# Kernel tuning notes

Measured on AMD Instinct MI355X. Metric: run time of the kernel, lower is better.

## Reference

```python
import jax, jax.numpy as jnp
import numpy as np

N, E, D_IN, D_OUT = 100000, 1250000, 64, 100


def setup_inputs() -> dict:
    key = jax.random.key(0)
    ks = jax.random.split(key, 12)
    inp = {
        "x": jax.random.normal(ks[0], (N, D_IN), dtype=jnp.float32),
        "edge_index": jax.random.randint(ks[1], (2, E), 0, N, dtype=jnp.int64),
        "edge_weight": jax.random.uniform(ks[2], (E,), dtype=jnp.float32),
        # ChebConv(64,100,K=1): one weight + bias
        "W10": jax.random.normal(ks[3], (D_IN, D_OUT), dtype=jnp.float32) * 0.1,
        "b1": jnp.zeros((D_OUT,), dtype=jnp.float32),
        # ChebConv(64,100,K=2)
        "W20": jax.random.normal(ks[4], (D_IN, D_OUT), dtype=jnp.float32) * 0.1,
        "W21": jax.random.normal(ks[5], (D_IN, D_OUT), dtype=jnp.float32) * 0.1,
        "b2": jnp.zeros((D_OUT,), dtype=jnp.float32),
        # ChebConv(64,100,K=3)
        "W30": jax.random.normal(ks[6], (D_IN, D_OUT), dtype=jnp.float32) * 0.1,
        "W31": jax.random.normal(ks[7], (D_IN, D_OUT), dtype=jnp.float32) * 0.1,
        "W32": jax.random.normal(ks[8], (D_IN, D_OUT), dtype=jnp.float32) * 0.1,
        "b3": jnp.zeros((D_OUT,), dtype=jnp.float32),
    }
    return inp


def _cheb_norm(edge_index, edge_weight, n):
    # PyG ChebConv.__norm__ with normalization='sym', lambda_max=2.0:
    # L_hat = (2/lambda_max) * (I - D^-1/2 A D^-1/2) - I = -D^-1/2 A D^-1/2
    # (the +1 diagonal of L and the -1 self-loop cancel), diag entries are 0.
    row, col = edge_index[0], edge_index[1]
    deg = jax.ops.segment_sum(edge_weight, row, num_segments=n)
    dis = jnp.where(deg > 0, jax.lax.rsqrt(jnp.where(deg > 0, deg, 1.0)), 0.0)
    return -dis[row] * edge_weight * dis[col]


def _cheb_conv(x, edge_index, w_hat, weights, bias):
    # out = sum_k T_k(L_hat) x @ W_k + b, with T0=x, T1=Lx, T_k=2L T_{k-1}-T_{k-2}
    n = x.shape[0]
    row, col = edge_index[0], edge_index[1]

    def prop(t):  # L_hat @ t via edge gather/scatter
        return jax.ops.segment_sum(t[row] * w_hat[:, None], col, num_segments=n)

    tx0 = x
    out = tx0 @ weights[0]
    if len(weights) > 1:
        tx1 = prop(tx0)
        out = out + tx1 @ weights[1]
        for k in range(2, len(weights)):
            tx2 = 2.0 * prop(tx1) - tx0
            out = out + tx2 @ weights[k]
            tx0, tx1 = tx1, tx2
    return out + bias


def reference(x, edge_index, edge_weight, W10, b1, W20, W21, b2, W30, W31, W32, b3):
    w_hat = _cheb_norm(edge_index, edge_weight, x.shape[0])
    s1 = _cheb_conv(x, edge_index, w_hat, [W10], b1)
    s2 = _cheb_conv(x, edge_index, w_hat, [W20, W21], b2)
    s3 = _cheb_conv(x, edge_index, w_hat, [W30, W31, W32], b3)
    return jnp.concatenate([s1, s2, s3], axis=1)  # [N, 300]
```

## Files before the change

### kernel.cpp

```cpp
#include <hip/hip_runtime.h>


typedef __attribute__((ext_vector_type(8))) short short8;
typedef __attribute__((ext_vector_type(8))) unsigned short ushort8;
typedef __attribute__((ext_vector_type(4))) float f32x4;

#define NSBMAX 64
#define NSPLIT 16

__device__ inline float bf2f(unsigned short u) {
    return __uint_as_float(((unsigned int)u) << 16);
}
__device__ inline unsigned short f2bf(float f) {
    unsigned int u = __float_as_uint(f);
    u = (u + 0x7FFF + ((u >> 16) & 1)) >> 16;
    return (unsigned short)u;
}

__global__ __launch_bounds__(512) void partA_kernel(
        const int* __restrict__ row, const int* __restrict__ col,
        const float* __restrict__ ew, int* __restrict__ colAcur,
        int* __restrict__ rowAcur, uint2* __restrict__ colA,
        uint2* __restrict__ rowA, int E, int nsb, int chunk, int capA) {
    __shared__ int hc[NSBMAX];
    __shared__ int hr[NSBMAX];
    const int t = threadIdx.x;
    const int s = blockIdx.x * chunk;
    const int e = min(E, s + chunk);
    if (s >= E) return;
    if (t < NSBMAX) { hc[t] = 0; hr[t] = 0; }
    __syncthreads();
    for (int i = s + t; i < e; i += 512) {
        atomicAdd(&hc[col[i] >> 11], 1);
        atomicAdd(&hr[row[i] >> 11], 1);
    }
    __syncthreads();
    if (t < nsb) {
        int n = hc[t];
        hc[t] = n ? atomicAdd(&colAcur[t], n) : 0;
        n = hr[t];
        hr[t] = n ? atomicAdd(&rowAcur[t], n) : 0;
    }
    __syncthreads();
    for (int i = s + t; i < e; i += 512) {
        int r = row[i], c = col[i];
        float w = ew[i];
        int pc = atomicAdd(&hc[c >> 11], 1);
        if (pc < capA)
            colA[(size_t)(c >> 11) * capA + pc] =
                make_uint2(((unsigned)(c & 2047) << 17) | (unsigned)r, __float_as_uint(w));
        int pr = atomicAdd(&hr[r >> 11], 1);
        if (pr < capA)
            rowA[(size_t)(r >> 11) * capA + pr] = make_uint2((unsigned)r, __float_as_uint(w));
    }
}

__global__ __launch_bounds__(512) void partB_kernel(
        const int* __restrict__ colAcur, const uint2* __restrict__ colA,
        int* __restrict__ colBcur, uint2* __restrict__ colB,
        int capA, int capB) {
    __shared__ int h[8];
    const int sb = blockIdx.x / NSPLIT;
    const int j = blockIdx.x % NSPLIT;
    const int t = threadIdx.x;
    const int cnt = min(colAcur[sb], capA);
    const int chunk = (cnt + NSPLIT - 1) / NSPLIT;
    const int s = j * chunk;
    const int e = min(cnt, s + chunk);
    if (t < 8) h[t] = 0;
    __syncthreads();
    const uint2* part = colA + (size_t)sb * capA;
    for (int i = s + t; i < e; i += 512) atomicAdd(&h[part[i].x >> 25], 1);
    __syncthreads();
    if (t < 8) {
        int n = h[t];
        h[t] = n ? atomicAdd(&colBcur[sb * 8 + t], n) : 0;
    }
    __syncthreads();
    for (int i = s + t; i < e; i += 512) {
        uint2 rec = part[i];
        int f = rec.x >> 25;
        int p = atomicAdd(&h[f], 1);
        if (p < capB) {
            unsigned coff = (rec.x >> 17) & 255u;
            unsigned r = rec.x & 0x1FFFFu;
            colB[(size_t)(sb * 8 + f) * capB + p] = make_uint2((coff << 24) | r, rec.y);
        }
    }
}

__global__ __launch_bounds__(512) void fine_rowp_kernel(
        const int* __restrict__ rowAcur, const uint2* __restrict__ rowA,
        float* __restrict__ partial, int capA) {
    __shared__ float sdeg[2048];
    const int sb = blockIdx.x / NSPLIT;
    const int j = blockIdx.x % NSPLIT;
    const int t = threadIdx.x;
    const int cnt = min(rowAcur[sb], capA);
    const int chunk = (cnt + NSPLIT - 1) / NSPLIT;
    const int s = j * chunk;
    const int e = min(cnt, s + chunk);
    for (int k = t; k < 2048; k += 512) sdeg[k] = 0.f;
    __syncthreads();
    const uint2* part = rowA + (size_t)sb * capA;
    for (int i = s + t; i < e; i += 512) {
        uint2 rec = part[i];
        atomicAdd(&sdeg[rec.x & 2047u], __uint_as_float(rec.y));
    }
    __syncthreads();
    float* dstp = partial + (size_t)blockIdx.x * 2048;
    for (int k = t; k < 2048; k += 512) dstp[k] = sdeg[k];
}

__global__ void colbase_scan_kernel(const int* __restrict__ colBcur,
                                    int* __restrict__ colbase,
                                    int* __restrict__ rowptr, int N, int nfb, int capB) {
    __shared__ int s[512];
    int t = threadIdx.x;
    int v = (t < nfb) ? min(colBcur[t], capB) : 0;
    s[t] = v;
    __syncthreads();
    for (int o = 1; o < 512; o <<= 1) {
        int u = (t >= o) ? s[t - o] : 0;
        __syncthreads();
        s[t] += u;
        __syncthreads();
    }
    if (t < nfb) colbase[t] = s[t] - v;
    if (t == 511) rowptr[N] = s[511];
}

__global__ __launch_bounds__(256) void fine_col_kernel(
        const int* __restrict__ colBcur, const int* __restrict__ colbase,
        const uint2* __restrict__ colB, const float* __restrict__ dis,
        uint2* __restrict__ erec, int* __restrict__ rowptr, int N, int capB) {
    __shared__ int h[256];
    __shared__ int sc[256];
    __shared__ int cur[256];
    const int b = blockIdx.x, t = threadIdx.x;
    const int sz = min(colBcur[b], capB);
    const uint2* part = colB + (size_t)b * capB;
    h[t] = 0;
    __syncthreads();
    for (int i = t; i < sz; i += 256) atomicAdd(&h[part[i].x >> 24], 1);
    __syncthreads();
    int v = h[t];
    sc[t] = v;
    __syncthreads();
    for (int o = 1; o < 256; o <<= 1) {
        int u = (t >= o) ? sc[t - o] : 0;
        __syncthreads();
        sc[t] += u;
        __syncthreads();
    }
    int excl = sc[t] - v;
    const int base = colbase[b];
    int c = (b << 8) + t;
    if (c < N) rowptr[c] = base + excl;
    cur[t] = excl;
    __syncthreads();
    for (int i = t; i < sz; i += 256) {
        uint2 rec = part[i];
        int coff = rec.x >> 24;
        int r = rec.x & 0xFFFFFFu;
        int pos = atomicAdd(&cur[coff], 1);
        float wd = __uint_as_float(rec.y) * dis[r];
        erec[(size_t)base + pos] = make_uint2((unsigned)r, __float_as_uint(wd));
    }
}

__global__ void deg_count_kernel(const int* __restrict__ row, const int* __restrict__ col,
                                 const float* __restrict__ ew,
                                 float* __restrict__ deg, int* __restrict__ cnt, int E) {
    int e = blockIdx.x * 256 + threadIdx.x;
    if (e < E) {
        atomicAdd(&deg[row[e]], ew[e]);
        atomicAdd(&cnt[col[e]], 1);
    }
}

__global__ void scan1_kernel(const int* __restrict__ cnt, int* __restrict__ pre,
                             int* __restrict__ bsum, int N) {
    __shared__ int s[256];
    int t = threadIdx.x;
    int i = blockIdx.x * 256 + t;
    int v = (i < N) ? cnt[i] : 0;
    s[t] = v;
    __syncthreads();
    for (int o = 1; o < 256; o <<= 1) {
        int u = (t >= o) ? s[t - o] : 0;
        __syncthreads();
        s[t] += u;
        __syncthreads();
    }
    if (i < N) pre[i] = s[t] - v;
    if (t == 255) bsum[blockIdx.x] = s[255];
}

__global__ void scan2_kernel(const int* __restrict__ bsum, int* __restrict__ bpre, int nb) {
    __shared__ int s[512];
    int t = threadIdx.x;
    int v = (t < nb) ? bsum[t] : 0;
    s[t] = v;
    __syncthreads();
    for (int o = 1; o < 512; o <<= 1) {
        int u = (t >= o) ? s[t - o] : 0;
        __syncthreads();
        s[t] += u;
        __syncthreads();
    }
    if (t < nb) bpre[t] = s[t] - v;
}

__global__ void scan3_kernel(int* __restrict__ rowptr, int* __restrict__ cursor,
                             const int* __restrict__ bpre, int N, int E) {
    int i = blockIdx.x * 256 + threadIdx.x;
    if (i < N) {
        int v = rowptr[i] + bpre[i >> 8];
        rowptr[i] = v;
        cursor[i] = v;
    }
    if (i == 0) rowptr[N] = E;
}

__global__ void scatter_compact_kernel(const int* __restrict__ row, const int* __restrict__ col,
                                       const float* __restrict__ ew, int* __restrict__ cursor,
                                       uint2* __restrict__ erec, int E) {
    int e = blockIdx.x * 256 + threadIdx.x;
    if (e < E) {
        int p = atomicAdd(&cursor[col[e]], 1);
        erec[p] = make_uint2((unsigned)row[e], __float_as_uint(ew[e]));
    }
}

__global__ void cvt_dis_kernel(const float* __restrict__ x, unsigned short* __restrict__ xb,
                               const float* __restrict__ degp, float* __restrict__ dis,
                               int N, int total4, int mode) {
    int i = blockIdx.x * 256 + threadIdx.x;
    if (i < total4) {
        float4 v = reinterpret_cast<const float4*>(x)[i];
        ushort4 o;
        o.x = f2bf(v.x); o.y = f2bf(v.y); o.z = f2bf(v.z); o.w = f2bf(v.w);
        reinterpret_cast<ushort4*>(xb)[i] = o;
    }
    if (mode && i < N) {
        float d;
        if (mode == 2) {
            const float* p = degp + ((size_t)(i >> 11) * NSPLIT) * 2048 + (i & 2047);
            d = 0.f;
#pragma unroll
            for (int j = 0; j < NSPLIT; ++j) d += p[(size_t)j * 2048];
        } else {
            d = degp[i];
        }
        dis[i] = (d > 0.f) ? rsqrtf(d) : 0.f;
    }
}

__global__ void gather_kernel(const int* __restrict__ ptr, const uint2* __restrict__ erec,
                              const float* __restrict__ dis,
                              const unsigned short* __restrict__ src,
                              unsigned short* __restrict__ dst, int N, int premul) {
    int node = blockIdx.x * 4 + (threadIdx.x >> 6);
    int lane = threadIdx.x & 63;
    if (node >= N) return;
    int s = ptr[node];
    int d = ptr[node + 1] - s;
    float acc = 0.f;
    for (int base = 0; base < d; base += 64) {
        int n = min(64, d - base);
        int ex = 0;
        float w = 0.f;
        if (lane < n) {
            uint2 e = erec[s + base + lane];
            ex = (int)e.x;
            w = __uint_as_float(e.y);
            if (!premul) w *= dis[ex];
        }
        int n4 = (n + 3) & ~3;
        for (int j = 0; j < n4; j += 4) {
            int r0 = __shfl(ex, j + 0, 64);
            int r1 = __shfl(ex, j + 1, 64);
            int r2 = __shfl(ex, j + 2, 64);
            int r3 = __shfl(ex, j + 3, 64);
            float w0 = __shfl(w, j + 0, 64);
            float w1 = __shfl(w, j + 1, 64);
            float w2 = __shfl(w, j + 2, 64);
            float w3 = __shfl(w, j + 3, 64);
            float v0 = bf2f(src[(size_t)r0 * 64 + lane]);
            float v1 = bf2f(src[(size_t)r1 * 64 + lane]);
            float v2 = bf2f(src[(size_t)r2 * 64 + lane]);
            float v3 = bf2f(src[(size_t)r3 * 64 + lane]);
            acc = fmaf(w0, v0, acc);
            acc = fmaf(w1, v1, acc);
            acc = fmaf(w2, v2, acc);
            acc = fmaf(w3, v3, acc);
        }
    }
    dst[(size_t)node * 64 + lane] = f2bf(-dis[node] * acc);
}

__global__ void prep_w_kernel(const float* __restrict__ W10, const float* __restrict__ W20,
                              const float* __restrict__ W21, const float* __restrict__ W30,
                              const float* __restrict__ W31, const float* __restrict__ W32,
                              unsigned short* __restrict__ imgW) {
    int i = blockIdx.x * 256 + threadIdx.x;
    if (i >= 6 * 7168) return;
    int img = i / 7168;
    int rem = i - img * 7168;
    int colc = rem >> 6;
    int k = rem & 63;
    const float* W;
    switch (img) {
        case 0: W = W10; break;
        case 1: W = W20; break;
        case 2: W = W21; break;
        case 3: W = W30; break;
        case 4: W = W31; break;
        default: W = W32; break;
    }
    float v = (colc < 100) ? W[k * 100 + colc] : 0.f;
    int g = k >> 3, j = k & 7;
    imgW[img * 7168 + colc * 64 + ((g ^ (colc & 7)) << 3) + j] = f2bf(v);
}

__global__ __launch_bounds__(256) void gemm_mfma_kernel(
        const unsigned short* __restrict__ xb, const unsigned short* __restrict__ tx1b,
        const unsigned short* __restrict__ p2b, const unsigned short* __restrict__ imgW,
        const float* __restrict__ b1, const float* __restrict__ b2,
        const float* __restrict__ b3, float* __restrict__ out, int N) {
    __shared__ unsigned short Ft[64 * 64];
    __shared__ unsigned short Ws[112 * 64];
    const int bid = blockIdx.x;
    const int seg = bid % 3;
    const int tile = bid / 3;
    const int row0 = tile * 64;
    const int tid = threadIdx.x;
    const int wv = tid >> 6;
    const int l = tid & 63;
    const int m = l & 15;
    const int q = l >> 4;

    f32x4 acc[7];
#pragma unroll
    for (int t = 0; t < 7; ++t) acc[t] = (f32x4){0.f, 0.f, 0.f, 0.f};

    const int imgBase = (seg * (seg + 1) / 2) * 7168;

    for (int c = 0; c <= seg; ++c) {
        const unsigned short* __restrict__ src = (c == 0) ? xb : (c == 1) ? tx1b : p2b;
#pragma unroll
        for (int it = 0; it < 2; ++it) {
            int i = tid + it * 256;
            int r = i >> 3, g = i & 7;
            int grow = row0 + r;
            ushort8 v = {0, 0, 0, 0, 0, 0, 0, 0};
            if (grow < N) {
                v = *reinterpret_cast<const ushort8*>(src + (size_t)grow * 64 + g * 8);
                if (c == 2) {
                    ushort8 xv = *reinterpret_cast<const ushort8*>(xb + (size_t)grow * 64 + g * 8);
#pragma unroll
                    for (int jj = 0; jj < 8; ++jj)
                        v[jj] = f2bf(2.f * bf2f(v[jj]) - bf2f(xv[jj]));
                }
            }
            *reinterpret_cast<ushort8*>(&Ft[r * 64 + ((g ^ (r & 7)) << 3)]) = v;
        }
        const uint4* wsrc = reinterpret_cast<const uint4*>(imgW + imgBase + c * 7168);
        uint4* wdst = reinterpret_cast<uint4*>(Ws);
#pragma unroll
        for (int it = 0; it < 4; ++it) {
            int i = tid + it * 256;
            if (i < 896) wdst[i] = wsrc[i];
        }
        __syncthreads();

        const int arow = wv * 16 + m;
#pragma unroll
        for (int ks = 0; ks < 2; ++ks) {
            short8 a = *reinterpret_cast<const short8*>(
                &Ft[arow * 64 + (((ks * 4 + q) ^ (arow & 7)) << 3)]);
#pragma unroll
            for (int t = 0; t < 7; ++t) {
                int n = t * 16 + m;
                short8 b = *reinterpret_cast<const short8*>(
                    &Ws[n * 64 + (((ks * 4 + q) ^ (n & 7)) << 3)]);
                acc[t] = __builtin_amdgcn_mfma_f32_16x16x32_bf16(a, b, acc[t], 0, 0, 0);
            }
        }
        __syncthreads();
    }

    const float* bsel = (seg == 0) ? b1 : (seg == 1) ? b2 : b3;
#pragma unroll
    for (int t = 0; t < 7; ++t) {
        int colseg = t * 16 + m;
        if (colseg >= 100) continue;
        float bv = bsel[colseg];
#pragma unroll
        for (int i = 0; i < 4; ++i) {
            int grow = row0 + wv * 16 + q * 4 + i;
            if (grow < N) out[(size_t)grow * 300 + seg * 100 + colseg] = acc[t][i] + bv;
        }
    }
}

extern "C" void kernel_launch(void* const* d_in, const int* in_sizes, int n_in,
                              void* d_out, int out_size, void* d_ws, size_t ws_size,
                              hipStream_t stream) {
    const float* x   = (const float*)d_in[0];
    const int*   ei  = (const int*)d_in[1];
    const float* ew  = (const float*)d_in[2];
    const float* W10 = (const float*)d_in[3];
    const float* b1  = (const float*)d_in[4];
    const float* W20 = (const float*)d_in[5];
    const float* W21 = (const float*)d_in[6];
    const float* b2  = (const float*)d_in[7];
    const float* W30 = (const float*)d_in[8];
    const float* W31 = (const float*)d_in[9];
    const float* W32 = (const float*)d_in[10];
    const float* b3  = (const float*)d_in[11];
    float* out = (float*)d_out;

    const int N = in_sizes[0] / 64;
    const int E = in_sizes[2];
    const int* row = ei;
    const int* col = ei + E;
    const int nb = (N + 255) / 256;
    const int eb = (E + 255) / 256;

    const int NSB = (N + 2047) >> 11;
    const int nfb = NSB * 8;

    int total4 = N * 16;
    int pg = (N + 3) / 4;
    int ntile = (N + 63) / 64;

    long meanA = ((long)E * 2048 + N - 1) / N;
    int capA = (int)(meanA + meanA / 4 + 1024);
    long meanB = ((long)E * 256 + N - 1) / N;
    int capB = (int)(meanB + meanB / 4 + 512);

    char* base = (char*)d_ws;
    size_t off = 0;
    auto alloc = [&](size_t bytes) { size_t o = off; off = (off + bytes + 15) & ~(size_t)15; return o; };

    float* dis           = (float*)(base + alloc((size_t)4 * N));
    int*   rowptr        = (int*)(base + alloc((size_t)4 * (N + 1)));
    int*   colAcur       = (int*)(base + alloc((size_t)4 * 640));
    int*   rowAcur       = colAcur + 64;
    int*   colBcur       = colAcur + 128;
    int*   colbase       = (int*)(base + alloc((size_t)4 * 512));
    unsigned short* xb   = (unsigned short*)(base + alloc((size_t)128 * N));
    unsigned short* tx1b = (unsigned short*)(base + alloc((size_t)128 * N));
    unsigned short* p2b  = (unsigned short*)(base + alloc((size_t)128 * N));
    unsigned short* imgW = (unsigned short*)(base + alloc((size_t)2 * 6 * 7168));
    uint2* erec          = (uint2*)(base + alloc((size_t)8 * E));
    size_t mainfix = off;
    uint2* colA          = (uint2*)(base + alloc((size_t)8 * NSB * capA));
    uint2* rowA          = (uint2*)(base + alloc((size_t)8 * NSB * capA));
    uint2* colB          = (uint2*)(base + alloc((size_t)8 * nfb * capB));
    float* partial       = (float*)(base + alloc((size_t)4 * NSB * NSPLIT * 2048));
    size_t mainneed = off;

    bool mainok = (N <= 131072) && (NSB <= NSBMAX) && (nfb <= 512) && (mainneed <= ws_size);

    if (mainok) {
        const int PBLK = 512;
        int chunkA = (E + PBLK - 1) / PBLK;

        hipMemsetAsync(colAcur, 0, (size_t)4 * 640, stream);
        partA_kernel<<<PBLK, 512, 0, stream>>>(row, col, ew, colAcur, rowAcur,
                                               colA, rowA, E, NSB, chunkA, capA);
        partB_kernel<<<NSB * NSPLIT, 512, 0, stream>>>(colAcur, colA, colBcur, colB,
                                                       capA, capB);
        fine_rowp_kernel<<<NSB * NSPLIT, 512, 0, stream>>>(rowAcur, rowA, partial, capA);
        cvt_dis_kernel<<<(total4 + 255) / 256, 256, 0, stream>>>(x, xb, partial, dis,
                                                                 N, total4, 2);
        colbase_scan_kernel<<<1, 512, 0, stream>>>(colBcur, colbase, rowptr, N, nfb, capB);
        fine_col_kernel<<<nfb, 256, 0, stream>>>(colBcur, colbase, colB, dis,
                                                 erec, rowptr, N, capB);
        prep_w_kernel<<<(6 * 7168 + 255) / 256, 256, 0, stream>>>(W10, W20, W21, W30, W31, W32, imgW);

        gather_kernel<<<pg, 256, 0, stream>>>(rowptr, erec, dis, xb, tx1b, N, 1);
        gather_kernel<<<pg, 256, 0, stream>>>(rowptr, erec, dis, tx1b, p2b, N, 1);
        gemm_mfma_kernel<<<ntile * 3, 256, 0, stream>>>(xb, tx1b, p2b, imgW, b1, b2, b3, out, N);
    } else {
        off = mainfix;
        float* deg    = (float*)(base + alloc((size_t)4 * N));
        int*   cursor = (int*)(base + alloc((size_t)4 * N));
        int*   bsum   = (int*)(base + alloc((size_t)4 * nb));
        int*   bpre   = (int*)(base + alloc((size_t)4 * nb));

        hipMemsetAsync(deg, 0, (size_t)4 * N, stream);
        hipMemsetAsync(cursor, 0, (size_t)4 * N, stream);
        deg_count_kernel<<<eb, 256, 0, stream>>>(row, col, ew, deg, cursor, E);
        scan1_kernel<<<nb, 256, 0, stream>>>(cursor, rowptr, bsum, N);
        scan2_kernel<<<1, 512, 0, stream>>>(bsum, bpre, nb);
        scan3_kernel<<<nb, 256, 0, stream>>>(rowptr, cursor, bpre, N, E);
        scatter_compact_kernel<<<eb, 256, 0, stream>>>(row, col, ew, cursor, erec, E);
        cvt_dis_kernel<<<(total4 + 255) / 256, 256, 0, stream>>>(x, xb, deg, dis, N, total4, 1);
        prep_w_kernel<<<(6 * 7168 + 255) / 256, 256, 0, stream>>>(W10, W20, W21, W30, W31, W32, imgW);

        gather_kernel<<<pg, 256, 0, stream>>>(rowptr, erec, dis, xb, tx1b, N, 0);
        gather_kernel<<<pg, 256, 0, stream>>>(rowptr, erec, dis, tx1b, p2b, N, 0);
        gemm_mfma_kernel<<<ntile * 3, 256, 0, stream>>>(xb, tx1b, p2b, imgW, b1, b2, b3, out, N);
    }
}
```

Measured before the change: 386.5 us.

## Fuse three ChebConv GEMM segments into one block per row tile

Replaces the per-segment GEMM launch (three blocks per 64-row tile) with a single block that loads x, Tx1 and Tx2 once into shared memory and accumulates all six weight products into 21 accumulators. Weights are repacked in MFMA fragment order so B operands are read directly from global/L2 instead of being staged in LDS. This removes redundant loads of x and Tx1 across segments and the weight LDS copies and syncs, at the cost of much higher register pressure (84 accumulator VGPRs plus A fragments) and fewer blocks, which may reduce occupancy.

```diff
diff --git a/kernel.cpp b/kernel.cpp
--- a/kernel.cpp
+++ b/kernel.cpp
@@ -308,8 +308,10 @@
     if (i >= 6 * 7168) return;
     int img = i / 7168;
     int rem = i - img * 7168;
-    int colc = rem >> 6;
-    int k = rem & 63;
+    int j = rem & 7;
+    int l = (rem >> 3) & 63;
+    int ks = (rem >> 9) & 1;
+    int t = rem >> 10;
     const float* W;
     switch (img) {
         case 0: W = W10; break;
@@ -319,88 +321,96 @@
         case 4: W = W31; break;
         default: W = W32; break;
     }
-    float v = (colc < 100) ? W[k * 100 + colc] : 0.f;
-    int g = k >> 3, j = k & 7;
-    imgW[img * 7168 + colc * 64 + ((g ^ (colc & 7)) << 3) + j] = f2bf(v);
-}
-
-__global__ __launch_bounds__(256) void gemm_mfma_kernel(
+    int n = t * 16 + (l & 15);
+    int k = ks * 32 + (l >> 4) * 8 + j;
+    float v = (n < 100) ? W[k * 100 + n] : 0.f;
+    imgW[i] = f2bf(v);
+}
+
+#define PRODUCT(AF, IMGOFF, SEGBASE)                                                   \
+    do {                                                                               \
+        _Pragma("unroll") for (int ks = 0; ks < 2; ++ks) {                             \
+            _Pragma("unroll") for (int t = 0; t < 7; ++t) {                            \
+                short8 bfr = *reinterpret_cast<const short8*>(                         \
+                    imgW + (IMGOFF) + ((t * 2 + ks) << 9) + (l << 3));                 \
+                acc[(SEGBASE) + t] = __builtin_amdgcn_mfma_f32_16x16x32_bf16(          \
+                    AF[ks], bfr, acc[(SEGBASE) + t], 0, 0, 0);                         \
+            }                                                                          \
+        }                                                                              \
+    } while (0)
+
+__global__ __launch_bounds__(256) void gemm_fused_kernel(
         const unsigned short* __restrict__ xb, const unsigned short* __restrict__ tx1b,
         const unsigned short* __restrict__ p2b, const unsigned short* __restrict__ imgW,
         const float* __restrict__ b1, const float* __restrict__ b2,
         const float* __restrict__ b3, float* __restrict__ out, int N) {
-    __shared__ unsigned short Ft[64 * 64];
-    __shared__ unsigned short Ws[112 * 64];
-    const int bid = blockIdx.x;
-    const int seg = bid % 3;
-    const int tile = bid / 3;
-    const int row0 = tile * 64;
+    __shared__ unsigned short Ftx[64 * 64];
+    __shared__ unsigned short Ft1[64 * 64];
+    __shared__ unsigned short Ft2[64 * 64];
+    const int row0 = blockIdx.x * 64;
     const int tid = threadIdx.x;
     const int wv = tid >> 6;
     const int l = tid & 63;
     const int m = l & 15;
     const int q = l >> 4;
 
-    f32x4 acc[7];
-#pragma unroll
-    for (int t = 0; t < 7; ++t) acc[t] = (f32x4){0.f, 0.f, 0.f, 0.f};
-
-    const int imgBase = (seg * (seg + 1) / 2) * 7168;
-
-    for (int c = 0; c <= seg; ++c) {
-        const unsigned short* __restrict__ src = (c == 0) ? xb : (c == 1) ? tx1b : p2b;
-#pragma unroll
-        for (int it = 0; it < 2; ++it) {
-            int i = tid + it * 256;
-            int r = i >> 3, g = i & 7;
-            int grow = row0 + r;
-            ushort8 v = {0, 0, 0, 0, 0, 0, 0, 0};
-            if (grow < N) {
-                v = *reinterpret_cast<const ushort8*>(src + (size_t)grow * 64 + g * 8);
-                if (c == 2) {
-                    ushort8 xv = *reinterpret_cast<const ushort8*>(xb + (size_t)grow * 64 + g * 8);
-#pragma unroll
-                    for (int jj = 0; jj < 8; ++jj)
-                        v[jj] = f2bf(2.f * bf2f(v[jj]) - bf2f(xv[jj]));
-                }
+    f32x4 acc[21];
+#pragma unroll
+    for (int t = 0; t < 21; ++t) acc[t] = (f32x4){0.f, 0.f, 0.f, 0.f};
+
+#pragma unroll
+    for (int it = 0; it < 2; ++it) {
+        int i = tid + it * 256;
+        int r = i >> 3, g = i & 7;
+        int grow = row0 + r;
+        ushort8 vx = {0, 0, 0, 0, 0, 0, 0, 0};
+        ushort8 v1 = vx, v2 = vx;
+        if (grow < N) {
+            vx = *reinterpret_cast<const ushort8*>(xb + (size_t)grow * 64 + g * 8);
+            v1 = *reinterpret_cast<const ushort8*>(tx1b + (size_t)grow * 64 + g * 8);
+            ushort8 vp = *reinterpret_cast<const ushort8*>(p2b + (size_t)grow * 64 + g * 8);
+#pragma unroll
+            for (int jj = 0; jj < 8; ++jj)
+                v2[jj] = f2bf(2.f * bf2f(vp[jj]) - bf2f(vx[jj]));
+        }
+        int off = r * 64 + ((g ^ (r & 7)) << 3);
+        *reinterpret_cast<ushort8*>(&Ftx[off]) = vx;
+        *reinterpret_cast<ushort8*>(&Ft1[off]) = v1;
+        *reinterpret_cast<ushort8*>(&Ft2[off]) = v2;
+    }
+    __syncthreads();
+
+    const int arow = wv * 16 + m;
+    short8 ax[2], a1[2], a2[2];
+#pragma unroll
+    for (int ks = 0; ks < 2; ++ks) {
+        int o = arow * 64 + (((ks * 4 + q) ^ (arow & 7)) << 3);
+        ax[ks] = *reinterpret_cast<const short8*>(&Ftx[o]);
+        a1[ks] = *reinterpret_cast<const short8*>(&Ft1[o]);
+        a2[ks] = *reinterpret_cast<const short8*>(&Ft2[o]);
+    }
+
+    PRODUCT(ax, 0, 0);
+    PRODUCT(ax, 7168, 7);
+    PRODUCT(a1, 14336, 7);
+    PRODUCT(ax, 21504, 14);
+    PRODUCT(a1, 28672, 14);
+    PRODUCT(a2, 35840, 14);
+
+#pragma unroll
+    for (int seg = 0; seg < 3; ++seg) {
+        const float* bs = (seg == 0) ? b1 : (seg == 1) ? b2 : b3;
+#pragma unroll
+        for (int t = 0; t < 7; ++t) {
+            int colseg = t * 16 + m;
+            if (colseg >= 100) continue;
+            float bv = bs[colseg];
+#pragma unroll
+            for (int i = 0; i < 4; ++i) {
+                int grow = row0 + wv * 16 + q * 4 + i;
+                if (grow < N)
+                    out[(size_t)grow * 300 + seg * 100 + colseg] = acc[seg * 7 + t][i] + bv;
             }
-            *reinterpret_cast<ushort8*>(&Ft[r * 64 + ((g ^ (r & 7)) << 3)]) = v;
-        }
-        const uint4* wsrc = reinterpret_cast<const uint4*>(imgW + imgBase + c * 7168);
-        uint4* wdst = reinterpret_cast<uint4*>(Ws);
-#pragma unroll
-        for (int it = 0; it < 4; ++it) {
-            int i = tid + it * 256;
-            if (i < 896) wdst[i] = wsrc[i];
-        }
-        __syncthreads();
-
-        const int arow = wv * 16 + m;
-#pragma unroll
-        for (int ks = 0; ks < 2; ++ks) {
-            short8 a = *reinterpret_cast<const short8*>(
-                &Ft[arow * 64 + (((ks * 4 + q) ^ (arow & 7)) << 3)]);
-#pragma unroll
-            for (int t = 0; t < 7; ++t) {
-                int n = t * 16 + m;
-                short8 b = *reinterpret_cast<const short8*>(
-                    &Ws[n * 64 + (((ks * 4 + q) ^ (n & 7)) << 3)]);
-                acc[t] = __builtin_amdgcn_mfma_f32_16x16x32_bf16(a, b, acc[t], 0, 0, 0);
-            }
-        }
-        __syncthreads();
-    }
-
-    const float* bsel = (seg == 0) ? b1 : (seg == 1) ? b2 : b3;
-#pragma unroll
-    for (int t = 0; t < 7; ++t) {
-        int colseg = t * 16 + m;
-        if (colseg >= 100) continue;
-        float bv = bsel[colseg];
-#pragma unroll
-        for (int i = 0; i < 4; ++i) {
-            int grow = row0 + wv * 16 + q * 4 + i;
-            if (grow < N) out[(size_t)grow * 300 + seg * 100 + colseg] = acc[t][i] + bv;
         }
     }
 }
@@ -484,7 +494,7 @@
 
         gather_kernel<<<pg, 256, 0, stream>>>(rowptr, erec, dis, xb, tx1b, N, 1);
         gather_kernel<<<pg, 256, 0, stream>>>(rowptr, erec, dis, tx1b, p2b, N, 1);
-        gemm_mfma_kernel<<<ntile * 3, 256, 0, stream>>>(xb, tx1b, p2b, imgW, b1, b2, b3, out, N);
+        gemm_fused_kernel<<<ntile, 256, 0, stream>>>(xb, tx1b, p2b, imgW, b1, b2, b3, out, N);
     } else {
         off = mainfix;
         float* deg    = (float*)(base + alloc((size_t)4 * N));
@@ -504,6 +514,6 @@
 
         gather_kernel<<<pg, 256, 0, stream>>>(rowptr, erec, dis, xb, tx1b, N, 0);
         gather_kernel<<<pg, 256, 0, stream>>>(rowptr, erec, dis, tx1b, p2b, N, 0);
-        gemm_mfma_kernel<<<ntile * 3, 256, 0, stream>>>(xb, tx1b, p2b, imgW, b1, b2, b3, out, N);
-    }
-}
+        gemm_fused_kernel<<<ntile, 256, 0, stream>>>(xb, tx1b, p2b, imgW, b1, b2, b3, out, N);
+    }
+}
```

Measured after the change: 403.9 us. 4.5% more time.
